# Kernel optimization log

Measured on AMD Instinct MI355X. Metric: run time of the kernel, lower is better.

## Reference

```python
import jax, jax.numpy as jnp
import numpy as np

# Equal-sized graph batches (batch vectors are sorted, contiguous segments)
B, NX, NY = 16, 1024, 4096   # clouds, coarse pts/cloud, fine pts/cloud
C, CS, H = 256, 128, 256     # coarse feat dim, skip feat dim, MLP hidden
EPS = 1e-8


def setup_inputs() -> dict:
    key = jax.random.key(0)
    ks = jax.random.split(key, 8)
    x = jax.random.normal(ks[0], (B * NX, C), dtype=jnp.float32)
    pos = jax.random.normal(ks[1], (B * NX, 3), dtype=jnp.float32)
    x_skip = jax.random.normal(ks[2], (B * NY, CS), dtype=jnp.float32)
    pos_skip = jax.random.normal(ks[3], (B * NY, 3), dtype=jnp.float32)
    batch = jnp.repeat(jnp.arange(B, dtype=jnp.int32), NX)
    batch_skip = jnp.repeat(jnp.arange(B, dtype=jnp.int32), NY)
    W1 = jax.random.normal(ks[4], (C + CS, H), dtype=jnp.float32) * 0.05
    b1 = jnp.zeros((H,), dtype=jnp.float32)
    W2 = jax.random.normal(ks[5], (H, H), dtype=jnp.float32) * 0.05
    b2 = jnp.zeros((H,), dtype=jnp.float32)
    return {"x": x, "pos": pos, "batch": batch, "x_skip": x_skip,
            "pos_skip": pos_skip, "batch_skip": batch_skip,
            "W1": W1, "b1": b1, "W2": W2, "b2": b2, "k": 3}


def knn_interpolate(x, pos, pos_skip, k):
    # Reshape flat batched point sets into [B, n, .] (batch vectors are
    # contiguous equal-sized segments, so this matches the per-batch loop).
    fx = x.reshape(B, NX, C)
    px = pos.reshape(B, NX, 3)
    py = pos_skip.reshape(B, NY, 3)
    # Squared distances via the Gram trick: [B, NY, NX]
    d2 = (jnp.sum(py * py, -1)[:, :, None]
          + jnp.sum(px * px, -1)[:, None, :]
          - 2.0 * jnp.einsum('byd,bxd->byx', py, px))
    neg_d2, idx = jax.lax.top_k(-d2, k)            # k nearest (smallest d2)
    dist = jnp.sqrt(jnp.maximum(-neg_d2, 0.0))     # [B, NY, k]
    w = 1.0 / (dist + EPS)
    gathered = jax.vmap(lambda f, i: f[i])(fx, idx)  # [B, NY, k, C]
    num = jnp.einsum('byk,bykc->byc', w, gathered)
    den = jnp.sum(w, axis=-1, keepdims=True) + EPS
    return (num / den).reshape(B * NY, C)


def reference(x, pos, batch, x_skip, pos_skip, batch_skip, W1, b1, W2, b2, k):
    interp = knn_interpolate(x, pos, pos_skip, k)      # [B*NY, C]
    h = jnp.concatenate([interp, x_skip], axis=1)      # [B*NY, C+CS]
    h = jax.nn.relu(h @ W1 + b1)
    h = jax.nn.relu(h @ W2 + b2)
    return h
```

## Files before the change

kernel.cpp:

```cpp
#include <hip/hip_runtime.h>
#include <hip/hip_bf16.h>

#define B_  16
#define NX_ 1024
#define NY_ 4096
#define C_  256
#define CS_ 128
#define H_  256
#define M_  (B_ * NY_)
#define K1_ (C_ + CS_)
#define K2_ (H_)

using short8  = __attribute__((ext_vector_type(8))) short;
using floatx4 = __attribute__((ext_vector_type(4))) float;

__device__ __forceinline__ unsigned short f2bf(float f) {
    unsigned int u = __float_as_uint(f);
    unsigned int r = (u + 0x7fffu + ((u >> 16) & 1u)) >> 16;
    return (unsigned short)r;
}

typedef const __attribute__((address_space(1))) void gas_t;
typedef __attribute__((address_space(3))) void las_t;
__device__ __forceinline__ void gload_lds16(const void* g, void* l) {
    __builtin_amdgcn_global_load_lds((gas_t*)g, (las_t*)l, 16, 0, 0);
}

__global__ __launch_bounds__(256) void knn_select(
    const float* __restrict__ pos, const float* __restrict__ pos_skip,
    int4* __restrict__ idx4, float4* __restrict__ wgt4)
{
    __shared__ float4 sp[NX_];
    __shared__ float  md[3][3][64];
    __shared__ int    mi[3][3][64];

    const int tid = threadIdx.x;
    const int q   = tid >> 6;
    const int p   = tid & 63;
    const int y   = blockIdx.x * 64 + p;
    const int b   = y >> 12;

    for (int j = tid; j < NX_; j += 256) {
        const float* pp = pos + (size_t)(b * NX_ + j) * 3;
        float px = pp[0], py = pp[1], pz = pp[2];
        float pn = __fadd_rn(__fadd_rn(__fmul_rn(px, px), __fmul_rn(py, py)),
                             __fmul_rn(pz, pz));
        sp[j] = make_float4(px, py, pz, pn);
    }
    __syncthreads();

    const float* qp = pos_skip + (size_t)y * 3;
    const float qx = qp[0], qy = qp[1], qz = qp[2];
    const float qn = __fadd_rn(__fadd_rn(__fmul_rn(qx, qx), __fmul_rn(qy, qy)),
                               __fmul_rn(qz, qz));

    float d0 = 3.4e38f, d1 = 3.4e38f, d2 = 3.4e38f;
    int   n0 = 0x7fffffff, n1 = 0x7fffffff, n2 = 0x7fffffff;
    const int j0 = q * 256;
    #pragma unroll 8
    for (int t = 0; t < 256; ++t) {
        const int j = j0 + t;
        const float4 pv = sp[j];
        float dot = __fadd_rn(__fadd_rn(__fmul_rn(qx, pv.x),
                                        __fmul_rn(qy, pv.y)),
                              __fmul_rn(qz, pv.z));
        float dd = __fsub_rn(__fadd_rn(qn, pv.w), __fmul_rn(2.0f, dot));
        if (dd < d2) {
            if (dd < d1) {
                d2 = d1; n2 = n1;
                if (dd < d0) { d1 = d0; n1 = n0; d0 = dd; n0 = j; }
                else         { d1 = dd; n1 = j; }
            } else { d2 = dd; n2 = j; }
        }
    }

    if (q != 0) {
        md[q - 1][0][p] = d0; md[q - 1][1][p] = d1; md[q - 1][2][p] = d2;
        mi[q - 1][0][p] = n0; mi[q - 1][1][p] = n1; mi[q - 1][2][p] = n2;
    }
    __syncthreads();

    if (q == 0) {
        #pragma unroll
        for (int m = 0; m < 3; ++m) {
            const float b0 = md[m][0][p], b1 = md[m][1][p], b2 = md[m][2][p];
            const int  ib0 = mi[m][0][p], ib1 = mi[m][1][p], ib2 = mi[m][2][p];
            const float a0 = d0, a1 = d1, a2 = d2;
            const int  ia0 = n0, ia1 = n1, ia2 = n2;
            if (a0 <= b0) {
                d0 = a0; n0 = ia0;
                if (a1 <= b0) { d1 = a1; n1 = ia1;
                    bool c = (a2 <= b0); d2 = c ? a2 : b0; n2 = c ? ia2 : ib0; }
                else          { d1 = b0; n1 = ib0;
                    bool c = (a1 <= b1); d2 = c ? a1 : b1; n2 = c ? ia1 : ib1; }
            } else {
                d0 = b0; n0 = ib0;
                if (a0 <= b1) { d1 = a0; n1 = ia0;
                    bool c = (a1 <= b1); d2 = c ? a1 : b1; n2 = c ? ia1 : ib1; }
                else          { d1 = b1; n1 = ib1;
                    bool c = (a0 <= b2); d2 = c ? a0 : b2; n2 = c ? ia0 : ib2; }
            }
        }
        const float w0 = 1.0f / (sqrtf(fmaxf(d0, 0.0f)) + 1e-8f);
        const float w1 = 1.0f / (sqrtf(fmaxf(d1, 0.0f)) + 1e-8f);
        const float w2 = 1.0f / (sqrtf(fmaxf(d2, 0.0f)) + 1e-8f);
        const float inv_den = 1.0f / (w0 + w1 + w2 + 1e-8f);
        idx4[y] = make_int4(n0, n1, n2, 0);
        wgt4[y] = make_float4(w0, w1, w2, inv_den);
    }
}

__global__ __launch_bounds__(256) void gather_concat(
    const float* __restrict__ x, const float* __restrict__ x_skip,
    const int4* __restrict__ idx4, const float4* __restrict__ wgt4,
    unsigned short* __restrict__ h0)
{
    const int wave = threadIdx.x >> 6, lane = threadIdx.x & 63;
    const int y = blockIdx.x * 4 + wave;
    const int4  id = idx4[y];
    const float4 w = wgt4[y];
    const float* fb = x + (size_t)(y >> 12) * (NX_ * C_);

    const float4 f0 = *(const float4*)(fb + (size_t)id.x * C_ + lane * 4);
    const float4 f1 = *(const float4*)(fb + (size_t)id.y * C_ + lane * 4);
    const float4 f2 = *(const float4*)(fb + (size_t)id.z * C_ + lane * 4);

    ushort4 o;
    o.x = f2bf((w.x * f0.x + w.y * f1.x + w.z * f2.x) * w.w);
    o.y = f2bf((w.x * f0.y + w.y * f1.y + w.z * f2.y) * w.w);
    o.z = f2bf((w.x * f0.z + w.y * f1.z + w.z * f2.z) * w.w);
    o.w = f2bf((w.x * f0.w + w.y * f1.w + w.z * f2.w) * w.w);
    *(ushort4*)(h0 + (size_t)y * K1_ + lane * 4) = o;

    const float2 s2 = *(const float2*)(x_skip + (size_t)y * CS_ + lane * 2);
    ushort2 os; os.x = f2bf(s2.x); os.y = f2bf(s2.y);
    *(ushort2*)(h0 + (size_t)y * K1_ + C_ + lane * 2) = os;
}

__global__ __launch_bounds__(256) void prep_w(
    const float* __restrict__ W1, const float* __restrict__ W2,
    unsigned short* __restrict__ W1t, unsigned short* __restrict__ W2t)
{
    int id = blockIdx.x * 256 + threadIdx.x;
    if (id < K1_ * H_) {
        int n = id / K1_, k = id - n * K1_;
        W1t[id] = f2bf(W1[(size_t)k * H_ + n]);
    }
    if (id < K2_ * H_) {
        int n = id >> 8, k = id & 255;
        W2t[id] = f2bf(W2[(size_t)k * H_ + n]);
    }
}

template<int K, int OUT_BF16>
__global__ __launch_bounds__(256) void gemm_bias_relu(
    const unsigned short* __restrict__ A,
    const unsigned short* __restrict__ Bt,
    const float* __restrict__ bias,
    void* __restrict__ outp)
{
    __shared__ unsigned short As[2][64 * 64];
    __shared__ unsigned short Bs[2][256 * 64];

    const int tid  = threadIdx.x;
    const int lane = tid & 63;
    const int wave = tid >> 6;
    const int m0   = blockIdx.x * 64;
    const int r16  = lane & 15, qk = lane >> 4;

    floatx4 acc[4][4] = {};

    auto stage = [&](int buf, int kt) {
        #pragma unroll
        for (int i = 0; i < 2; ++i) {
            const int row  = (tid >> 3) + i * 32;
            const int slot = (tid & 7) ^ (row & 7);
            gload_lds16(A + (size_t)(m0 + row) * K + kt + slot * 8,
                        &As[buf][row * 64 + (tid & 7) * 8]);
        }
        #pragma unroll
        for (int i = 0; i < 8; ++i) {
            const int row  = (tid >> 3) + i * 32;
            const int slot = (tid & 7) ^ (row & 7);
            gload_lds16(Bt + (size_t)row * K + kt + slot * 8,
                        &Bs[buf][row * 64 + (tid & 7) * 8]);
        }
    };

    auto compute = [&](int buf) {
        #pragma unroll
        for (int s = 0; s < 2; ++s) {
            short8 af[4], bf[4];
            #pragma unroll
            for (int m = 0; m < 4; ++m) {
                const int row  = m * 16 + r16;
                const int slot = (s * 4 + qk) ^ (r16 & 7);
                af[m] = *(const short8*)&As[buf][row * 64 + slot * 8];
            }
            #pragma unroll
            for (int n = 0; n < 4; ++n) {
                const int row  = wave * 64 + n * 16 + r16;
                const int slot = (s * 4 + qk) ^ (r16 & 7);
                bf[n] = *(const short8*)&Bs[buf][row * 64 + slot * 8];
            }
            #pragma unroll
            for (int m = 0; m < 4; ++m)
                #pragma unroll
                for (int n = 0; n < 4; ++n)
                    acc[m][n] = __builtin_amdgcn_mfma_f32_16x16x32_bf16(
                        af[m], bf[n], acc[m][n], 0, 0, 0);
        }
    };

    stage(0, 0);
    __syncthreads();
    int cur = 0;
    constexpr int NT = K / 64;
    #pragma unroll
    for (int t = 1; t < NT; ++t) {
        stage(cur ^ 1, t * 64);
        compute(cur);
        __syncthreads();
        cur ^= 1;
    }
    compute(cur);

    #pragma unroll
    for (int n = 0; n < 4; ++n) {
        const int gc = wave * 64 + n * 16 + r16;
        const float bv = bias[gc];
        #pragma unroll
        for (int m = 0; m < 4; ++m) {
            #pragma unroll
            for (int r = 0; r < 4; ++r) {
                const int gr = m0 + m * 16 + qk * 4 + r;
                float v = fmaxf(acc[m][n][r] + bv, 0.0f);
                if (OUT_BF16)
                    ((unsigned short*)outp)[(size_t)gr * H_ + gc] = f2bf(v);
                else
                    ((float*)outp)[(size_t)gr * H_ + gc] = v;
            }
        }
    }
}

extern "C" void kernel_launch(void* const* d_in, const int* in_sizes, int n_in,
                              void* d_out, int out_size, void* d_ws, size_t ws_size,
                              hipStream_t stream)
{
    const float* x        = (const float*)d_in[0];
    const float* pos      = (const float*)d_in[1];
    const float* x_skip   = (const float*)d_in[3];
    const float* pos_skip = (const float*)d_in[4];
    const float* W1       = (const float*)d_in[6];
    const float* b1       = (const float*)d_in[7];
    const float* W2       = (const float*)d_in[8];
    const float* b2       = (const float*)d_in[9];

    char* ws = (char*)d_ws;
    unsigned short* h0  = (unsigned short*)(ws);
    unsigned short* h1  = (unsigned short*)(ws + 50331648);
    unsigned short* W1t = (unsigned short*)(ws + 83886080);
    unsigned short* W2t = (unsigned short*)(ws + 84082688);
    int4*           idx4 = (int4*)(ws + 84213760);
    float4*         wgt4 = (float4*)(ws + 85262336);

    hipLaunchKernelGGL(knn_select, dim3(M_ / 64), dim3(256), 0, stream,
                       pos, pos_skip, idx4, wgt4);
    hipLaunchKernelGGL(gather_concat, dim3(M_ / 4), dim3(256), 0, stream,
                       x, x_skip, idx4, wgt4, h0);
    hipLaunchKernelGGL(prep_w, dim3((K1_ * H_ + 255) / 256), dim3(256), 0, stream,
                       W1, W2, W1t, W2t);
    hipLaunchKernelGGL((gemm_bias_relu<K1_, 1>), dim3(M_ / 64), dim3(256),
                       0, stream, h0, W1t, b1, h1);
    hipLaunchKernelGGL((gemm_bias_relu<K2_, 0>), dim3(M_ / 64), dim3(256),
                       0, stream, h1, W2t, b2, (float*)d_out);
}
```

Before: 214.3 us.

## Fuse kNN gather/concat into first GEMM and split kNN scan eight ways

The gather-interpolate-concat step is folded into the first GEMM kernel. It now builds the full 64x384 bf16 A tile in shared memory straight from x and x_skip, so the h0 intermediate is never written to or read back from global memory. The B tile for W1 is now single-buffered and staged between two barriers, which loses the old load/compute overlap. Separately, knn_select now splits each query's scan over 8 groups of 32 threads instead of 4 of 64, which adds blocks and makes a longer merge.

```diff
diff --git a/kernel.cpp b/kernel.cpp
--- a/kernel.cpp
+++ b/kernel.cpp
@@ -31,13 +31,13 @@
     int4* __restrict__ idx4, float4* __restrict__ wgt4)
 {
     __shared__ float4 sp[NX_];
-    __shared__ float  md[3][3][64];
-    __shared__ int    mi[3][3][64];
+    __shared__ float  md[7][3][32];
+    __shared__ int    mi[7][3][32];
 
     const int tid = threadIdx.x;
-    const int q   = tid >> 6;
-    const int p   = tid & 63;
-    const int y   = blockIdx.x * 64 + p;
+    const int e   = tid >> 5;
+    const int p   = tid & 31;
+    const int y   = blockIdx.x * 32 + p;
     const int b   = y >> 12;
 
     for (int j = tid; j < NX_; j += 256) {
@@ -56,9 +56,9 @@
 
     float d0 = 3.4e38f, d1 = 3.4e38f, d2 = 3.4e38f;
     int   n0 = 0x7fffffff, n1 = 0x7fffffff, n2 = 0x7fffffff;
-    const int j0 = q * 256;
+    const int j0 = e * 128;
     #pragma unroll 8
-    for (int t = 0; t < 256; ++t) {
+    for (int t = 0; t < 128; ++t) {
         const int j = j0 + t;
         const float4 pv = sp[j];
         float dot = __fadd_rn(__fadd_rn(__fmul_rn(qx, pv.x),
@@ -74,15 +74,15 @@
         }
     }
 
-    if (q != 0) {
-        md[q - 1][0][p] = d0; md[q - 1][1][p] = d1; md[q - 1][2][p] = d2;
-        mi[q - 1][0][p] = n0; mi[q - 1][1][p] = n1; mi[q - 1][2][p] = n2;
+    if (e != 0) {
+        md[e - 1][0][p] = d0; md[e - 1][1][p] = d1; md[e - 1][2][p] = d2;
+        mi[e - 1][0][p] = n0; mi[e - 1][1][p] = n1; mi[e - 1][2][p] = n2;
     }
     __syncthreads();
 
-    if (q == 0) {
-        #pragma unroll
-        for (int m = 0; m < 3; ++m) {
+    if (e == 0) {
+        #pragma unroll
+        for (int m = 0; m < 7; ++m) {
             const float b0 = md[m][0][p], b1 = md[m][1][p], b2 = md[m][2][p];
             const int  ib0 = mi[m][0][p], ib1 = mi[m][1][p], ib2 = mi[m][2][p];
             const float a0 = d0, a1 = d1, a2 = d2;
@@ -110,33 +110,6 @@
     }
 }
 
-__global__ __launch_bounds__(256) void gather_concat(
-    const float* __restrict__ x, const float* __restrict__ x_skip,
-    const int4* __restrict__ idx4, const float4* __restrict__ wgt4,
-    unsigned short* __restrict__ h0)
-{
-    const int wave = threadIdx.x >> 6, lane = threadIdx.x & 63;
-    const int y = blockIdx.x * 4 + wave;
-    const int4  id = idx4[y];
-    const float4 w = wgt4[y];
-    const float* fb = x + (size_t)(y >> 12) * (NX_ * C_);
-
-    const float4 f0 = *(const float4*)(fb + (size_t)id.x * C_ + lane * 4);
-    const float4 f1 = *(const float4*)(fb + (size_t)id.y * C_ + lane * 4);
-    const float4 f2 = *(const float4*)(fb + (size_t)id.z * C_ + lane * 4);
-
-    ushort4 o;
-    o.x = f2bf((w.x * f0.x + w.y * f1.x + w.z * f2.x) * w.w);
-    o.y = f2bf((w.x * f0.y + w.y * f1.y + w.z * f2.y) * w.w);
-    o.z = f2bf((w.x * f0.z + w.y * f1.z + w.z * f2.z) * w.w);
-    o.w = f2bf((w.x * f0.w + w.y * f1.w + w.z * f2.w) * w.w);
-    *(ushort4*)(h0 + (size_t)y * K1_ + lane * 4) = o;
-
-    const float2 s2 = *(const float2*)(x_skip + (size_t)y * CS_ + lane * 2);
-    ushort2 os; os.x = f2bf(s2.x); os.y = f2bf(s2.y);
-    *(ushort2*)(h0 + (size_t)y * K1_ + C_ + lane * 2) = os;
-}
-
 __global__ __launch_bounds__(256) void prep_w(
     const float* __restrict__ W1, const float* __restrict__ W2,
     unsigned short* __restrict__ W1t, unsigned short* __restrict__ W2t)
@@ -152,15 +125,15 @@
     }
 }
 
-template<int K, int OUT_BF16>
-__global__ __launch_bounds__(256) void gemm_bias_relu(
-    const unsigned short* __restrict__ A,
+__global__ __launch_bounds__(256) void gemm1_fused(
+    const float* __restrict__ x, const float* __restrict__ x_skip,
+    const int4* __restrict__ idx4, const float4* __restrict__ wgt4,
     const unsigned short* __restrict__ Bt,
     const float* __restrict__ bias,
-    void* __restrict__ outp)
-{
-    __shared__ unsigned short As[2][64 * 64];
-    __shared__ unsigned short Bs[2][256 * 64];
+    unsigned short* __restrict__ outp)
+{
+    __shared__ unsigned short As_full[6 * 64 * 64];
+    __shared__ unsigned short Bs[256 * 64];
 
     const int tid  = threadIdx.x;
     const int lane = tid & 63;
@@ -168,26 +141,56 @@
     const int m0   = blockIdx.x * 64;
     const int r16  = lane & 15, qk = lane >> 4;
 
-    floatx4 acc[4][4] = {};
-
-    auto stage = [&](int buf, int kt) {
-        #pragma unroll
-        for (int i = 0; i < 2; ++i) {
-            const int row  = (tid >> 3) + i * 32;
-            const int slot = (tid & 7) ^ (row & 7);
-            gload_lds16(A + (size_t)(m0 + row) * K + kt + slot * 8,
-                        &As[buf][row * 64 + (tid & 7) * 8]);
-        }
+    auto stageB = [&](int kt) {
         #pragma unroll
         for (int i = 0; i < 8; ++i) {
             const int row  = (tid >> 3) + i * 32;
             const int slot = (tid & 7) ^ (row & 7);
-            gload_lds16(Bt + (size_t)row * K + kt + slot * 8,
-                        &Bs[buf][row * 64 + (tid & 7) * 8]);
+            gload_lds16(Bt + (size_t)row * K1_ + kt + slot * 8,
+                        &Bs[row * 64 + (tid & 7) * 8]);
         }
     };
 
-    auto compute = [&](int buf) {
+    stageB(0);
+
+    {
+        const int ks  = lane >> 4;
+        const int cs  = (lane * 4) & 63;
+        const int sl  = cs >> 3;
+        const int of  = cs & 7;
+        const int ks2  = 4 + (lane >> 5);
+        const int cs2  = (lane * 2) & 63;
+        const int sl2  = cs2 >> 3;
+        const int of2  = cs2 & 7;
+        #pragma unroll 4
+        for (int i = 0; i < 16; ++i) {
+            const int r  = wave * 16 + i;
+            const int gr = m0 + r;
+            const int4   id = idx4[gr];
+            const float4 wt = wgt4[gr];
+            const float* fb = x + (size_t)(gr >> 12) * (NX_ * C_);
+            const float4 f0 = *(const float4*)(fb + (size_t)id.x * C_ + lane * 4);
+            const float4 f1 = *(const float4*)(fb + (size_t)id.y * C_ + lane * 4);
+            const float4 f2 = *(const float4*)(fb + (size_t)id.z * C_ + lane * 4);
+            ushort4 o;
+            o.x = f2bf((wt.x * f0.x + wt.y * f1.x + wt.z * f2.x) * wt.w);
+            o.y = f2bf((wt.x * f0.y + wt.y * f1.y + wt.z * f2.y) * wt.w);
+            o.z = f2bf((wt.x * f0.z + wt.y * f1.z + wt.z * f2.z) * wt.w);
+            o.w = f2bf((wt.x * f0.w + wt.y * f1.w + wt.z * f2.w) * wt.w);
+            *(ushort4*)&As_full[ks * 4096 + r * 64 + (sl ^ (r & 7)) * 8 + of] = o;
+
+            const float2 s2 = *(const float2*)(x_skip + (size_t)gr * CS_ + lane * 2);
+            ushort2 os; os.x = f2bf(s2.x); os.y = f2bf(s2.y);
+            *(ushort2*)&As_full[ks2 * 4096 + r * 64 + (sl2 ^ (r & 7)) * 8 + of2] = os;
+        }
+    }
+    __syncthreads();
+
+    floatx4 acc[4][4] = {};
+
+    #pragma unroll
+    for (int t = 0; t < 6; ++t) {
+        const unsigned short* At = As_full + t * 4096;
         #pragma unroll
         for (int s = 0; s < 2; ++s) {
             short8 af[4], bf[4];
@@ -195,13 +198,13 @@
             for (int m = 0; m < 4; ++m) {
                 const int row  = m * 16 + r16;
                 const int slot = (s * 4 + qk) ^ (r16 & 7);
-                af[m] = *(const short8*)&As[buf][row * 64 + slot * 8];
+                af[m] = *(const short8*)&At[row * 64 + slot * 8];
             }
             #pragma unroll
             for (int n = 0; n < 4; ++n) {
                 const int row  = wave * 64 + n * 16 + r16;
                 const int slot = (s * 4 + qk) ^ (r16 & 7);
-                bf[n] = *(const short8*)&Bs[buf][row * 64 + slot * 8];
+                bf[n] = *(const short8*)&Bs[row * 64 + slot * 8];
             }
             #pragma unroll
             for (int m = 0; m < 4; ++m)
@@ -210,14 +213,93 @@
                     acc[m][n] = __builtin_amdgcn_mfma_f32_16x16x32_bf16(
                         af[m], bf[n], acc[m][n], 0, 0, 0);
         }
+        if (t < 5) {
+            __syncthreads();
+            stageB((t + 1) * 64);
+            __syncthreads();
+        }
+    }
+
+    #pragma unroll
+    for (int n = 0; n < 4; ++n) {
+        const int gc = wave * 64 + n * 16 + r16;
+        const float bv = bias[gc];
+        #pragma unroll
+        for (int m = 0; m < 4; ++m) {
+            #pragma unroll
+            for (int r = 0; r < 4; ++r) {
+                const int gr = m0 + m * 16 + qk * 4 + r;
+                float v = fmaxf(acc[m][n][r] + bv, 0.0f);
+                outp[(size_t)gr * H_ + gc] = f2bf(v);
+            }
+        }
+    }
+}
+
+__global__ __launch_bounds__(256) void gemm2_bias_relu(
+    const unsigned short* __restrict__ A,
+    const unsigned short* __restrict__ Bt,
+    const float* __restrict__ bias,
+    float* __restrict__ outp)
+{
+    __shared__ unsigned short As[2][64 * 64];
+    __shared__ unsigned short Bs[2][256 * 64];
+
+    const int tid  = threadIdx.x;
+    const int lane = tid & 63;
+    const int wave = tid >> 6;
+    const int m0   = blockIdx.x * 64;
+    const int r16  = lane & 15, qk = lane >> 4;
+
+    floatx4 acc[4][4] = {};
+
+    auto stage = [&](int buf, int kt) {
+        #pragma unroll
+        for (int i = 0; i < 2; ++i) {
+            const int row  = (tid >> 3) + i * 32;
+            const int slot = (tid & 7) ^ (row & 7);
+            gload_lds16(A + (size_t)(m0 + row) * K2_ + kt + slot * 8,
+                        &As[buf][row * 64 + (tid & 7) * 8]);
+        }
+        #pragma unroll
+        for (int i = 0; i < 8; ++i) {
+            const int row  = (tid >> 3) + i * 32;
+            const int slot = (tid & 7) ^ (row & 7);
+            gload_lds16(Bt + (size_t)row * K2_ + kt + slot * 8,
+                        &Bs[buf][row * 64 + (tid & 7) * 8]);
+        }
+    };
+
+    auto compute = [&](int buf) {
+        #pragma unroll
+        for (int s = 0; s < 2; ++s) {
+            short8 af[4], bf[4];
+            #pragma unroll
+            for (int m = 0; m < 4; ++m) {
+                const int row  = m * 16 + r16;
+                const int slot = (s * 4 + qk) ^ (r16 & 7);
+                af[m] = *(const short8*)&As[buf][row * 64 + slot * 8];
+            }
+            #pragma unroll
+            for (int n = 0; n < 4; ++n) {
+                const int row  = wave * 64 + n * 16 + r16;
+                const int slot = (s * 4 + qk) ^ (r16 & 7);
+                bf[n] = *(const short8*)&Bs[buf][row * 64 + slot * 8];
+            }
+            #pragma unroll
+            for (int m = 0; m < 4; ++m)
+                #pragma unroll
+                for (int n = 0; n < 4; ++n)
+                    acc[m][n] = __builtin_amdgcn_mfma_f32_16x16x32_bf16(
+                        af[m], bf[n], acc[m][n], 0, 0, 0);
+        }
     };
 
     stage(0, 0);
     __syncthreads();
     int cur = 0;
-    constexpr int NT = K / 64;
     #pragma unroll
-    for (int t = 1; t < NT; ++t) {
+    for (int t = 1; t < 4; ++t) {
         stage(cur ^ 1, t * 64);
         compute(cur);
         __syncthreads();
@@ -234,11 +316,7 @@
             #pragma unroll
             for (int r = 0; r < 4; ++r) {
                 const int gr = m0 + m * 16 + qk * 4 + r;
-                float v = fmaxf(acc[m][n][r] + bv, 0.0f);
-                if (OUT_BF16)
-                    ((unsigned short*)outp)[(size_t)gr * H_ + gc] = f2bf(v);
-                else
-                    ((float*)outp)[(size_t)gr * H_ + gc] = v;
+                outp[(size_t)gr * H_ + gc] = fmaxf(acc[m][n][r] + bv, 0.0f);
             }
         }
     }
@@ -258,21 +336,18 @@
     const float* b2       = (const float*)d_in[9];
 
     char* ws = (char*)d_ws;
-    unsigned short* h0  = (unsigned short*)(ws);
-    unsigned short* h1  = (unsigned short*)(ws + 50331648);
-    unsigned short* W1t = (unsigned short*)(ws + 83886080);
-    unsigned short* W2t = (unsigned short*)(ws + 84082688);
-    int4*           idx4 = (int4*)(ws + 84213760);
-    float4*         wgt4 = (float4*)(ws + 85262336);
-
-    hipLaunchKernelGGL(knn_select, dim3(M_ / 64), dim3(256), 0, stream,
+    unsigned short* h1  = (unsigned short*)(ws);
+    unsigned short* W1t = (unsigned short*)(ws + 33554432);
+    unsigned short* W2t = (unsigned short*)(ws + 33751040);
+    int4*           idx4 = (int4*)(ws + 33882112);
+    float4*         wgt4 = (float4*)(ws + 34930688);
+
+    hipLaunchKernelGGL(knn_select, dim3(M_ / 32), dim3(256), 0, stream,
                        pos, pos_skip, idx4, wgt4);
-    hipLaunchKernelGGL(gather_concat, dim3(M_ / 4), dim3(256), 0, stream,
-                       x, x_skip, idx4, wgt4, h0);
     hipLaunchKernelGGL(prep_w, dim3((K1_ * H_ + 255) / 256), dim3(256), 0, stream,
                        W1, W2, W1t, W2t);
-    hipLaunchKernelGGL((gemm_bias_relu<K1_, 1>), dim3(M_ / 64), dim3(256),
-                       0, stream, h0, W1t, b1, h1);
-    hipLaunchKernelGGL((gemm_bias_relu<K2_, 0>), dim3(M_ / 64), dim3(256),
-                       0, stream, h1, W2t, b2, (float*)d_out);
-}
+    hipLaunchKernelGGL(gemm1_fused, dim3(M_ / 64), dim3(256), 0, stream,
+                       x, x_skip, idx4, wgt4, W1t, b1, h1);
+    hipLaunchKernelGGL(gemm2_bias_relu, dim3(M_ / 64), dim3(256), 0, stream,
+                       h1, W2t, b2, (float*)d_out);
+}
```

Result: faster. 206.8 us (-3.5%).
